# Kernel optimization log

Hardware: AMD Instinct MI355X
Metric: run time of the kernel (lower is better)

## Reference

```python
import jax, jax.numpy as jnp
import numpy as np

N0, N1, N2 = 100000, 25000, 6250
E0, E1, E2 = 1600000, 400000, 100000
K = 6
NUM_CLASSES = 40


def cheb_conv(x, edge_index, W, b, num_nodes):
    # PyG ChebConv, normalization='sym', lambda_max=2.0:
    # L_hat = (2/lambda_max) * (I - D^-1/2 A D^-1/2) - I = -D^-1/2 A D^-1/2
    row, col = edge_index[0], edge_index[1]
    deg = jax.ops.segment_sum(jnp.ones(row.shape[0], x.dtype), row, num_segments=num_nodes)
    dinv = jnp.where(deg > 0, 1.0 / jnp.sqrt(jnp.maximum(deg, 1e-12)), 0.0)
    norm = -(dinv[row] * dinv[col])  # per-edge weight of L_hat

    def Lhat(v):  # [N, F] -> [N, F], sparse gather + scatter-add
        return jax.ops.segment_sum(norm[:, None] * v[col], row, num_segments=num_nodes)

    Tx0 = x
    out = Tx0 @ W[0]
    Tx1 = Lhat(x)
    out = out + Tx1 @ W[1]
    for k in range(2, W.shape[0]):  # Chebyshev recurrence T_k = 2 L_hat T_{k-1} - T_{k-2}
        Tx2 = 2.0 * Lhat(Tx1) - Tx0
        out = out + Tx2 @ W[k]
        Tx0, Tx1 = Tx1, Tx2
    return out + b


def spmm_pool(row, col, values, n_out, h):
    # torch_sparse.spmm(indices, values, size0, size1, h)
    return jax.ops.segment_sum(values[:, None] * h[col], row, num_segments=n_out)


def setup_inputs() -> dict:
    key = jax.random.key(0)
    ks = jax.random.split(key, 16)
    w = lambda k, shape: jax.random.normal(k, shape, jnp.float32) * 0.1
    return {
        "pos": jax.random.normal(ks[0], (N0, 3), jnp.float32),
        "edge_index0": jax.random.randint(ks[1], (2, E0), 0, N0),
        "edge_index1": jax.random.randint(ks[2], (2, E1), 0, N1),
        "edge_index2": jax.random.randint(ks[3], (2, E2), 0, N2),
        "ds0_row": jax.random.randint(ks[4], (N0,), 0, N1),
        "ds0_col": jax.random.randint(ks[5], (N0,), 0, N0),
        "ds0_values": jax.random.uniform(ks[6], (N0,), jnp.float32),
        "ds1_row": jax.random.randint(ks[7], (N1,), 0, N2),
        "ds1_col": jax.random.randint(ks[8], (N1,), 0, N1),
        "ds1_values": jax.random.uniform(ks[9], (N1,), jnp.float32),
        "W0": w(ks[10], (K, 3, 32)),  "b0": jnp.zeros((32,), jnp.float32),
        "W1": w(ks[11], (K, 32, 64)), "b1": jnp.zeros((64,), jnp.float32),
        "W2": w(ks[12], (K, 64, 128)),"b2": jnp.zeros((128,), jnp.float32),
        "Wh": w(ks[13], (128, 1024)), "bh": jnp.zeros((1024,), jnp.float32),
        "Wl": w(ks[14], (1024, NUM_CLASSES)), "bl": jnp.zeros((NUM_CLASSES,), jnp.float32),
    }


def reference(pos, edge_index0, edge_index1, edge_index2,
              ds0_row, ds0_col, ds0_values, ds1_row, ds1_col, ds1_values,
              W0, b0, W1, b1, W2, b2, Wh, bh, Wl, bl):
    h = jax.nn.relu(cheb_conv(pos, edge_index0, W0, b0, N0))
    h = spmm_pool(ds0_row, ds0_col, ds0_values, N1, h)
    h = jax.nn.relu(cheb_conv(h, edge_index1, W1, b1, N1))
    h = spmm_pool(ds1_row, ds1_col, ds1_values, N2, h)
    h = cheb_conv(h, edge_index2, W2, b2, N2)
    h = jnp.max(h @ Wh + bh, axis=0)  # global max pool over nodes
    return h @ Wl + bl  # [num_classes]
```

## Files before the change

### kernel.cpp

```cpp
#include <hip/hip_runtime.h>
#include <cstdint>
#include <cmath>

#define N0G 100000
#define N1G 25000
#define N2G 6250
#define E0G 1600000
#define E1G 400000
#define E2G 100000
#define KCH 6
#define NCLS 40
#define RPB 512
#define NBLK 240
#define PAYB 17
#define PAYM ((1u << PAYB) - 1u)
#define SCT 16
#define SCB (256 * SCT)
#define NST 5

static inline int cdiv(long a, long b){ return (int)((a + b - 1) / b); }

struct BP {
  const int* row[NST]; const int* col[NST]; const float* pval[NST];
  unsigned* ebuf[NST]; int* cs[NST]; float* wv[NST]; int* rp[NST]; float* dinv[NST];
  const float* xsrc[NST]; float4* xsdst[NST];
  int E[NST], N[NST], nbkt[NST], chunk[NST], ghoff[NST], pool[NST], nb[NST], bsumoff[NST];
  int blkS[NST + 1], blkB[NST + 1];
};

__global__ __launch_bounds__(256) void k_phist_b(BP p, int* __restrict__ gh){
  int s = blockIdx.x / NBLK, c = blockIdx.x % NBLK;
  const int* row = p.row[s];
  int E = p.E[s], nbkt = p.nbkt[s], chunk = p.chunk[s];
  int* g = gh + p.ghoff[s];
  __shared__ int h[256];
  for (int i = threadIdx.x; i < nbkt; i += 256) h[i] = 0;
  __syncthreads();
  int e0 = c * chunk, e1 = min(E, e0 + chunk);
  for (int e = e0 + threadIdx.x; e < e1; e += 256)
    atomicAdd(&h[row[e] >> 9], 1);
  __syncthreads();
  for (int i = threadIdx.x; i < nbkt; i += 256)
    g[i * NBLK + c] = h[i];
}

__global__ __launch_bounds__(256) void k_scanA_b(BP p, const int* __restrict__ gh, int* __restrict__ bsum){
  int s = 0; while (s < NST - 1 && (int)blockIdx.x >= p.blkS[s + 1]) s++;
  int lb = blockIdx.x - p.blkS[s];
  int M = p.nbkt[s] * NBLK;
  const int* g = gh + p.ghoff[s];
  __shared__ int sh[256];
  int base = lb * SCB + threadIdx.x * SCT;
  int su = 0;
#pragma unroll
  for (int j = 0; j < SCT; j++){ int i = base + j; if (i < M) su += g[i]; }
  sh[threadIdx.x] = su; __syncthreads();
  for (int o = 128; o > 0; o >>= 1){
    if (threadIdx.x < o) sh[threadIdx.x] += sh[threadIdx.x + o];
    __syncthreads();
  }
  if (threadIdx.x == 0) bsum[p.bsumoff[s] + lb] = sh[0];
}

__global__ __launch_bounds__(256) void k_scanC_b(BP p, int* __restrict__ gh, const int* __restrict__ bsum){
  int s = 0; while (s < NST - 1 && (int)blockIdx.x >= p.blkS[s + 1]) s++;
  int lb = blockIdx.x - p.blkS[s];
  int M = p.nbkt[s] * NBLK;
  int* g = gh + p.ghoff[s];
  __shared__ int sh[256];
  __shared__ int blockoff;
  if (threadIdx.x == 0){
    int off = 0;
    if (p.nb[s] > 1){
      const int* bs = bsum + p.bsumoff[s];
      for (int j = 0; j < lb; j++) off += bs[j];
    }
    blockoff = off;
  }
  int base = lb * SCB + threadIdx.x * SCT;
  int v[SCT]; int su = 0;
#pragma unroll
  for (int j = 0; j < SCT; j++){ int i = base + j; v[j] = (i < M) ? g[i] : 0; su += v[j]; }
  sh[threadIdx.x] = su;
  __syncthreads();
  for (int o = 1; o < 256; o <<= 1){
    int t = (threadIdx.x >= o) ? sh[threadIdx.x - o] : 0;
    __syncthreads();
    sh[threadIdx.x] += t;
    __syncthreads();
  }
  int excl = blockoff + sh[threadIdx.x] - su;
#pragma unroll
  for (int j = 0; j < SCT; j++){
    int i = base + j;
    if (i < M){ g[i] = excl; excl += v[j]; }
  }
  if (lb == 0 && threadIdx.x == 0) p.rp[s][p.N[s]] = p.E[s];
}

__global__ __launch_bounds__(256) void k_pscatter_b(BP p, const int* __restrict__ gh){
  int s = blockIdx.x / NBLK, c = blockIdx.x % NBLK;
  const int* row = p.row[s]; const int* col = p.col[s];
  int E = p.E[s], nbkt = p.nbkt[s], chunk = p.chunk[s], pool = p.pool[s];
  const int* g = gh + p.ghoff[s];
  unsigned* ebuf = p.ebuf[s];
  __shared__ int cur[256];
  for (int i = threadIdx.x; i < nbkt; i += 256) cur[i] = g[i * NBLK + c];
  __syncthreads();
  int e0 = c * chunk, e1 = min(E, e0 + chunk);
  for (int e = e0 + threadIdx.x; e < e1; e += 256){
    int r = row[e];
    int dst = atomicAdd(&cur[r >> 9], 1);
    unsigned pay = pool ? (unsigned)e : (unsigned)col[e];
    ebuf[dst] = ((unsigned)(r & 511) << PAYB) | pay;
  }
}

__global__ __launch_bounds__(512) void k_bfinal_b(BP p, const int* __restrict__ gh){
  int s = 0; while (s < NST - 1 && (int)blockIdx.x >= p.blkB[s + 1]) s++;
  int b = blockIdx.x - p.blkB[s];
  const int* g = gh + p.ghoff[s];
  const unsigned* ebuf = p.ebuf[s];
  int nbkt = p.nbkt[s], N = p.N[s], E = p.E[s], pool = p.pool[s];
  int* cs = p.cs[s]; float* wv = p.wv[s];
  int* rp = p.rp[s]; float* dinv = p.dinv[s];
  const int* pcol = p.col[s]; const float* pval = p.pval[s];
  __shared__ int h[512];
  __shared__ int cur[512];
  int e0 = g[b * NBLK];
  int e1 = (b + 1 < nbkt) ? g[(b + 1) * NBLK] : E;
  int r0 = b * RPB;
  int t = threadIdx.x;
  h[t] = 0;
  __syncthreads();
  for (int e = e0 + t; e < e1; e += 512)
    atomicAdd(&h[ebuf[e] >> PAYB], 1);
  __syncthreads();
  int cnt = h[t];
  __syncthreads();
  for (int o = 1; o < 512; o <<= 1){
    int tmp = (t >= o) ? h[t - o] : 0;
    __syncthreads();
    h[t] += tmp;
    __syncthreads();
  }
  int excl = h[t] - cnt;
  cur[t] = excl;
  int n = r0 + t;
  if (n < N){
    rp[n] = e0 + excl;
    if (!pool){
      float d = cnt > 0 ? rsqrtf((float)cnt) : 0.f;
      dinv[n] = d;
      if (p.xsrc[s]){
        const float* x = p.xsrc[s];
        p.xsdst[s][n] = make_float4(d * x[n * 3 + 0], d * x[n * 3 + 1], d * x[n * 3 + 2], 0.f);
      }
    }
  }
  __syncthreads();
  for (int e = e0 + t; e < e1; e += 512){
    unsigned u = ebuf[e];
    int pp = atomicAdd(&cur[u >> PAYB], 1);
    int dst = e0 + pp;
    if (pool){
      int ei = (int)(u & PAYM);
      cs[dst] = pcol[ei]; wv[dst] = pval[ei];
    } else {
      cs[dst] = (int)(u & PAYM);
    }
  }
}

__global__ __launch_bounds__(256) void k_gather3(const int* __restrict__ rp, const int* __restrict__ cs,
                          const float4* __restrict__ xs, const float* __restrict__ dinv,
                          const float* __restrict__ sub, float* __restrict__ dst,
                          float4* __restrict__ xs_out, int N, float scale){
  int tid = blockIdx.x * 256 + threadIdx.x;
  int n = tid >> 3, q = tid & 7;
  if (n >= N) return;
  int e0 = rp[n], e1 = rp[n + 1];
  float a0 = 0.f, a1 = 0.f, a2 = 0.f;
  for (int e = e0 + q; e < e1; e += 8){
    float4 v = xs[cs[e]];
    a0 += v.x; a1 += v.y; a2 += v.z;
  }
  a0 += __shfl_xor(a0, 1); a1 += __shfl_xor(a1, 1); a2 += __shfl_xor(a2, 1);
  a0 += __shfl_xor(a0, 2); a1 += __shfl_xor(a1, 2); a2 += __shfl_xor(a2, 2);
  a0 += __shfl_xor(a0, 4); a1 += __shfl_xor(a1, 4); a2 += __shfl_xor(a2, 4);
  if (q == 0){
    float dn = dinv[n];
    float m = -scale * dn;
    float r0 = m * a0, r1 = m * a1, r2 = m * a2;
    if (sub){ r0 -= sub[n * 3 + 0]; r1 -= sub[n * 3 + 1]; r2 -= sub[n * 3 + 2]; }
    dst[n * 3 + 0] = r0; dst[n * 3 + 1] = r1; dst[n * 3 + 2] = r2;
    if (xs_out) xs_out[n] = make_float4(dn * r0, dn * r1, dn * r2, 0.f);
  }
}

template<int F>
__global__ __launch_bounds__(256) void k_gatherT(const int* __restrict__ rp, const int* __restrict__ cs,
                          const float4* __restrict__ xs, const float* __restrict__ dinv,
                          const float* __restrict__ sub, float* __restrict__ dst,
                          float4* __restrict__ xs_out, int N, float scale){
  constexpr int L = F / 4;
  constexpr int G = 4 * L;
  int tid = blockIdx.x * 256 + threadIdx.x;
  int n = tid / G, q = tid % G;
  if (n >= N) return;
  int f4 = q % L, es = q / L;
  int e0 = rp[n], e1 = rp[n + 1];
  float4 acc = make_float4(0.f, 0.f, 0.f, 0.f);
  for (int e = e0 + es; e < e1; e += 4){
    float4 v = xs[(long)cs[e] * L + f4];
    acc.x += v.x; acc.y += v.y; acc.z += v.z; acc.w += v.w;
  }
  acc.x += __shfl_xor(acc.x, L);     acc.y += __shfl_xor(acc.y, L);
  acc.z += __shfl_xor(acc.z, L);     acc.w += __shfl_xor(acc.w, L);
  acc.x += __shfl_xor(acc.x, 2 * L); acc.y += __shfl_xor(acc.y, 2 * L);
  acc.z += __shfl_xor(acc.z, 2 * L); acc.w += __shfl_xor(acc.w, 2 * L);
  if (es == 0){
    float dn = dinv[n];
    float m = -scale * dn;
    float4 r = make_float4(m * acc.x, m * acc.y, m * acc.z, m * acc.w);
    if (sub){
      float4 sv = ((const float4*)sub)[(long)n * L + f4];
      r.x -= sv.x; r.y -= sv.y; r.z -= sv.z; r.w -= sv.w;
    }
    ((float4*)dst)[(long)n * L + f4] = r;
    if (xs_out) xs_out[(long)n * L + f4] = make_float4(dn * r.x, dn * r.y, dn * r.z, dn * r.w);
  }
}

template<int F>
__global__ __launch_bounds__(256) void k_gatherP(const int* __restrict__ rp, const int* __restrict__ cs,
                          const float* __restrict__ wv, const float* __restrict__ h,
                          float* __restrict__ dst, int N,
                          const float* __restrict__ dinvN, float4* __restrict__ xsN){
  constexpr int L = F / 4;
  int tid = blockIdx.x * 256 + threadIdx.x;
  int n = tid / L, q = tid % L;
  if (n >= N) return;
  const float4* h4 = (const float4*)h;
  int e0 = rp[n], e1 = rp[n + 1];
  float4 acc = make_float4(0.f, 0.f, 0.f, 0.f);
  for (int e = e0; e < e1; e++){
    int c = cs[e];
    float w = wv[e];
    float4 v = h4[(long)c * L + q];
    acc.x = fmaf(w, v.x, acc.x); acc.y = fmaf(w, v.y, acc.y);
    acc.z = fmaf(w, v.z, acc.z); acc.w = fmaf(w, v.w, acc.w);
  }
  ((float4*)dst)[(long)n * L + q] = acc;
  if (xsN){
    float dn = dinvN[n];
    xsN[(long)n * L + q] = make_float4(dn * acc.x, dn * acc.y, dn * acc.z, dn * acc.w);
  }
}

template<int F, int FO, int R, bool RELU>
__global__ __launch_bounds__(256) void k_cheb_tile(const float* __restrict__ x, const float* __restrict__ T, int N,
                           const float* __restrict__ W, const float* __restrict__ b,
                           float* __restrict__ out){
  constexpr int OQ4  = FO / 4;
  constexpr int NSUB = 256 / OQ4;
  constexpr int NT   = NSUB * R;
  constexpr int F6   = KCH * F;
  int n0 = blockIdx.x * NT;
  int o4   = threadIdx.x % OQ4;
  int nsub = threadIdx.x / OQ4;
  const float4* W4 = (const float4*)W;
  float4 acc[R];
  float4 bb = ((const float4*)b)[o4];
#pragma unroll
  for (int r = 0; r < R; r++) acc[r] = bb;

  if constexpr (F == 3){
    constexpr int PITCH = F6 + 2;
    __shared__ float X[NT * PITCH];
    for (int i = threadIdx.x; i < NT * F6; i += 256){
      int k = i / (NT * 3);
      int idx = i - k * (NT * 3);
      const float* src = (k == 0) ? x : (T + (size_t)(k - 1) * N * 3);
      int node = idx / 3, j = idx - node * 3;
      float v = (n0 + node < N) ? src[(long)n0 * 3 + idx] : 0.f;
      X[node * PITCH + k * 3 + j] = v;
    }
    __syncthreads();
#pragma unroll
    for (int f = 0; f < F6; f++){
      float4 w = W4[(long)f * OQ4 + o4];
#pragma unroll
      for (int r = 0; r < R; r++){
        float v = X[(nsub * R + r) * PITCH + f];
        acc[r].x = fmaf(v, w.x, acc[r].x); acc[r].y = fmaf(v, w.y, acc[r].y);
        acc[r].z = fmaf(v, w.z, acc[r].z); acc[r].w = fmaf(v, w.w, acc[r].w);
      }
    }
  } else {
    constexpr int L  = F / 4;
    constexpr int P4 = F6 / 4 + 1;
    __shared__ float4 X[NT * P4];
    for (int i = threadIdx.x; i < NT * KCH * L; i += 256){
      int k = i / (NT * L);
      int idx = i - k * (NT * L);
      int node = idx / L, q = idx - node * L;
      const float4* src4 = (const float4*)((k == 0) ? x : (T + (size_t)(k - 1) * N * F));
      float4 v = make_float4(0.f, 0.f, 0.f, 0.f);
      if (n0 + node < N) v = src4[(long)n0 * L + idx];
      X[node * P4 + k * L + q] = v;
    }
    __syncthreads();
#pragma unroll 4
    for (int f4 = 0; f4 < F6 / 4; f4++){
      float4 w0 = W4[(long)(4 * f4 + 0) * OQ4 + o4];
      float4 w1 = W4[(long)(4 * f4 + 1) * OQ4 + o4];
      float4 w2 = W4[(long)(4 * f4 + 2) * OQ4 + o4];
      float4 w3 = W4[(long)(4 * f4 + 3) * OQ4 + o4];
#pragma unroll
      for (int r = 0; r < R; r++){
        float4 hv = X[(nsub * R + r) * P4 + f4];
        acc[r].x = fmaf(hv.x, w0.x, acc[r].x); acc[r].y = fmaf(hv.x, w0.y, acc[r].y);
        acc[r].z = fmaf(hv.x, w0.z, acc[r].z); acc[r].w = fmaf(hv.x, w0.w, acc[r].w);
        acc[r].x = fmaf(hv.y, w1.x, acc[r].x); acc[r].y = fmaf(hv.y, w1.y, acc[r].y);
        acc[r].z = fmaf(hv.y, w1.z, acc[r].z); acc[r].w = fmaf(hv.y, w1.w, acc[r].w);
        acc[r].x = fmaf(hv.z, w2.x, acc[r].x); acc[r].y = fmaf(hv.z, w2.y, acc[r].y);
        acc[r].z = fmaf(hv.z, w2.z, acc[r].z); acc[r].w = fmaf(hv.z, w2.w, acc[r].w);
        acc[r].x = fmaf(hv.w, w3.x, acc[r].x); acc[r].y = fmaf(hv.w, w3.y, acc[r].y);
        acc[r].z = fmaf(hv.w, w3.z, acc[r].z); acc[r].w = fmaf(hv.w, w3.w, acc[r].w);
      }
    }
  }

#pragma unroll
  for (int r = 0; r < R; r++){
    int n = n0 + nsub * R + r;
    if (n < N){
      float4 o = acc[r];
      if (RELU){
        o.x = fmaxf(o.x, 0.f); o.y = fmaxf(o.y, 0.f);
        o.z = fmaxf(o.z, 0.f); o.w = fmaxf(o.w, 0.f);
      }
      ((float4*)out)[(long)n * OQ4 + o4] = o;
    }
  }
}

__device__ __forceinline__ unsigned fmap(float x){
  unsigned u = __float_as_uint(x);
  return (u & 0x80000000u) ? ~u : (u | 0x80000000u);
}
__device__ __forceinline__ float funmap(unsigned u){
  return (u & 0x80000000u) ? __uint_as_float(u ^ 0x80000000u) : __uint_as_float(~u);
}

#define NT 32
__global__ __launch_bounds__(256) void k_hidden_max(const float* __restrict__ h2, const float* __restrict__ Wh,
                             const float* __restrict__ bh, unsigned* __restrict__ maxed, int N){
  __shared__ float4 sW[128 * 32];
  __shared__ float4 sh4[NT * 32];
  const float4* Wh4 = (const float4*)Wh;
  int ob = blockIdx.x;
  for (int i = threadIdx.x; i < 128 * 32; i += 256){
    int f = i >> 5, ol = i & 31;
    sW[i] = Wh4[(long)f * 256 + ob * 32 + ol];
  }
  int o4l  = threadIdx.x & 31;
  int nsub = threadIdx.x >> 5;
  float4 mm = make_float4(-INFINITY, -INFINITY, -INFINITY, -INFINITY);
  int ntiles = (N + NT - 1) / NT;
  for (int nt = blockIdx.y; nt < ntiles; nt += gridDim.y){
    int n0 = nt * NT;
    __syncthreads();
    for (int i = threadIdx.x; i < NT * 32; i += 256){
      int n = i >> 5;
      float4 v = make_float4(0.f, 0.f, 0.f, 0.f);
      if (n0 + n < N) v = ((const float4*)h2)[(long)(n0 + n) * 32 + (i & 31)];
      sh4[i] = v;
    }
    __syncthreads();
    float4 acc[4];
#pragma unroll
    for (int j = 0; j < 4; j++) acc[j] = make_float4(0.f, 0.f, 0.f, 0.f);
#pragma unroll 4
    for (int f4 = 0; f4 < 32; f4++){
      float4 w0 = sW[(4 * f4 + 0) * 32 + o4l];
      float4 w1 = sW[(4 * f4 + 1) * 32 + o4l];
      float4 w2 = sW[(4 * f4 + 2) * 32 + o4l];
      float4 w3 = sW[(4 * f4 + 3) * 32 + o4l];
#pragma unroll
      for (int j = 0; j < 4; j++){
        float4 hv = sh4[(nsub * 4 + j) * 32 + f4];
        acc[j].x = fmaf(hv.x, w0.x, acc[j].x); acc[j].y = fmaf(hv.x, w0.y, acc[j].y);
        acc[j].z = fmaf(hv.x, w0.z, acc[j].z); acc[j].w = fmaf(hv.x, w0.w, acc[j].w);
        acc[j].x = fmaf(hv.y, w1.x, acc[j].x); acc[j].y = fmaf(hv.y, w1.y, acc[j].y);
        acc[j].z = fmaf(hv.y, w1.z, acc[j].z); acc[j].w = fmaf(hv.y, w1.w, acc[j].w);
        acc[j].x = fmaf(hv.z, w2.x, acc[j].x); acc[j].y = fmaf(hv.z, w2.y, acc[j].y);
        acc[j].z = fmaf(hv.z, w2.z, acc[j].z); acc[j].w = fmaf(hv.z, w2.w, acc[j].w);
        acc[j].x = fmaf(hv.w, w3.x, acc[j].x); acc[j].y = fmaf(hv.w, w3.y, acc[j].y);
        acc[j].z = fmaf(hv.w, w3.z, acc[j].z); acc[j].w = fmaf(hv.w, w3.w, acc[j].w);
      }
    }
#pragma unroll
    for (int j = 0; j < 4; j++){
      if (n0 + nsub * 4 + j < N){
        mm.x = fmaxf(mm.x, acc[j].x); mm.y = fmaxf(mm.y, acc[j].y);
        mm.z = fmaxf(mm.z, acc[j].z); mm.w = fmaxf(mm.w, acc[j].w);
      }
    }
  }
  __syncthreads();
  sh4[nsub * 32 + o4l] = mm;
  __syncthreads();
  if (nsub == 0){
#pragma unroll
    for (int s = 1; s < 8; s++){
      float4 o = sh4[s * 32 + o4l];
      mm.x = fmaxf(mm.x, o.x); mm.y = fmaxf(mm.y, o.y);
      mm.z = fmaxf(mm.z, o.z); mm.w = fmaxf(mm.w, o.w);
    }
    int o4 = ob * 32 + o4l;
    float4 b4 = ((const float4*)bh)[o4];
    atomicMax(&maxed[4 * o4 + 0], fmap(mm.x + b4.x));
    atomicMax(&maxed[4 * o4 + 1], fmap(mm.y + b4.y));
    atomicMax(&maxed[4 * o4 + 2], fmap(mm.z + b4.z));
    atomicMax(&maxed[4 * o4 + 3], fmap(mm.w + b4.w));
  }
}

__global__ __launch_bounds__(64) void k_final(const unsigned* __restrict__ maxed, const float* __restrict__ Wl,
                        const float* __restrict__ bl, float* __restrict__ out){
  int c = blockIdx.x;
  int l = threadIdx.x;
  float acc = 0.f;
  for (int o = l; o < 1024; o += 64)
    acc = fmaf(funmap(maxed[o]), Wl[o * NCLS + c], acc);
  for (int off = 32; off > 0; off >>= 1)
    acc += __shfl_down(acc, off);
  if (l == 0) out[c] = acc + bl[c];
}

template<int F, int FO, int R, bool RELU>
static void run_flowT(const int* rp, const int* cs, const float* dinv, int N,
                      const float* x, const float* W, const float* b, float* out,
                      float* T, float4* xin, float4* xout, hipStream_t s){
  const float* sub = nullptr; float scale = 1.f;
  const float* srcRaw = x;
  for (int k = 1; k < KCH; k++){
    float* Tk = T + (size_t)(k - 1) * N * F;
    float4* xo = (k == KCH - 1) ? nullptr : xout;
    k_gatherT<F><<<cdiv((long)N * F, 256), 256, 0, s>>>(rp, cs, xin, dinv, sub, Tk, xo, N, scale);
    sub = srcRaw; srcRaw = Tk; scale = 2.f;
    float4* t = xin; xin = xout; xout = t;
  }
  constexpr int NTC = (256 / (FO / 4)) * R;
  k_cheb_tile<F, FO, R, RELU><<<cdiv(N, NTC), 256, 0, s>>>(x, T, N, W, b, out);
}

extern "C" void kernel_launch(void* const* d_in, const int* in_sizes, int n_in,
                              void* d_out, int out_size, void* d_ws, size_t ws_size,
                              hipStream_t stream){
  const float* pos = (const float*)d_in[0];
  const int*   ei0 = (const int*)d_in[1];
  const int*   ei1 = (const int*)d_in[2];
  const int*   ei2 = (const int*)d_in[3];
  const int*   p0r = (const int*)d_in[4];
  const int*   p0c = (const int*)d_in[5];
  const float* p0v = (const float*)d_in[6];
  const int*   p1r = (const int*)d_in[7];
  const int*   p1c = (const int*)d_in[8];
  const float* p1v = (const float*)d_in[9];
  const float* W0  = (const float*)d_in[10]; const float* b0 = (const float*)d_in[11];
  const float* W1  = (const float*)d_in[12]; const float* b1 = (const float*)d_in[13];
  const float* W2  = (const float*)d_in[14]; const float* b2 = (const float*)d_in[15];
  const float* Wh  = (const float*)d_in[16]; const float* bh = (const float*)d_in[17];
  const float* Wl  = (const float*)d_in[18]; const float* bl = (const float*)d_in[19];
  float* out = (float*)d_out;

  float* TB = (float*)d_ws;
  float* hA = TB + 4000000;
  float* hB = hA + 3200000;
  float* hC = hB + 1600000;
  int* cs0   = (int*)(hC + 800000);
  int* cs1   = cs0 + 1600000;
  int* cs2   = cs1 + 400000;
  int* csP0  = cs2 + 100000;
  int* csP1  = csP0 + 100000;
  float* wvP0 = (float*)(csP1 + 25000);
  float* wvP1 = wvP0 + 100000;
  int* rp0  = (int*)(wvP1 + 25000);
  int* rp1  = rp0 + 100001;
  int* rp2  = rp1 + 25001;
  int* rpP0 = rp2 + 6251;
  int* rpP1 = rpP0 + 25001;
  float* dv0 = (float*)(rpP1 + 6251);
  float* dv1 = dv0 + 100000;
  float* dv2 = dv1 + 25000;
  int* gh   = (int*)(dv2 + 6250);
  int* bsum = gh + 76800;
  unsigned* maxed = (unsigned*)(bsum + 80);

  unsigned* eb0  = (unsigned*)TB;
  unsigned* eb1  = eb0 + 1600000;
  unsigned* eb2  = eb1 + 400000;
  unsigned* ebP0 = eb2 + 100000;
  unsigned* ebP1 = ebP0 + 100000;

  BP bp{};
  const int* rows[NST] = {ei0, ei1, ei2, p0r, p1r};
  const int* cols[NST] = {ei0 + E0G, ei1 + E1G, ei2 + E2G, p0c, p1c};
  const float* pvals[NST] = {nullptr, nullptr, nullptr, p0v, p1v};
  unsigned* ebufs[NST] = {eb0, eb1, eb2, ebP0, ebP1};
  int* css[NST] = {cs0, cs1, cs2, csP0, csP1};
  float* wvs[NST] = {nullptr, nullptr, nullptr, wvP0, wvP1};
  int* rps[NST] = {rp0, rp1, rp2, rpP0, rpP1};
  float* dvs[NST] = {dv0, dv1, dv2, nullptr, nullptr};
  int Es[NST] = {E0G, E1G, E2G, N0G, N1G};
  int Ns[NST] = {N0G, N1G, N2G, N1G, N2G};
  int pools[NST] = {0, 0, 0, 1, 1};
  int ghacc = 0, scanacc = 0, bacc = 0;
  bp.blkS[0] = 0; bp.blkB[0] = 0;
  for (int s = 0; s < NST; s++){
    bp.row[s] = rows[s]; bp.col[s] = cols[s]; bp.pval[s] = pvals[s];
    bp.ebuf[s] = ebufs[s]; bp.cs[s] = css[s]; bp.wv[s] = wvs[s];
    bp.rp[s] = rps[s]; bp.dinv[s] = dvs[s];
    bp.xsrc[s] = (s == 0) ? pos : nullptr;
    bp.xsdst[s] = (s == 0) ? (float4*)hB : nullptr;
    bp.E[s] = Es[s]; bp.N[s] = Ns[s]; bp.pool[s] = pools[s];
    bp.nbkt[s] = cdiv(Ns[s], RPB);
    bp.chunk[s] = cdiv(Es[s], NBLK);
    bp.ghoff[s] = ghacc; ghacc += bp.nbkt[s] * NBLK;
    bp.nb[s] = cdiv(bp.nbkt[s] * NBLK, SCB);
    bp.bsumoff[s] = s * 16;
    scanacc += bp.nb[s]; bp.blkS[s + 1] = scanacc;
    bacc += bp.nbkt[s]; bp.blkB[s + 1] = bacc;
  }

  k_phist_b<<<NST * NBLK, 256, 0, stream>>>(bp, gh);
  k_scanA_b<<<scanacc, 256, 0, stream>>>(bp, gh, bsum);
  k_scanC_b<<<scanacc, 256, 0, stream>>>(bp, gh, bsum);
  k_pscatter_b<<<NST * NBLK, 256, 0, stream>>>(bp, gh);
  k_bfinal_b<<<bacc, 512, 0, stream>>>(bp, gh);

  hipMemsetAsync(maxed, 0, 1024 * sizeof(unsigned), stream);

  {
    float4* xin = (float4*)hB; float4* xout = (float4*)(hB + 400000);
    const float* sub = nullptr; float scale = 1.f;
    const float* srcRaw = pos;
    for (int k = 1; k < KCH; k++){
      float* Tk = TB + (size_t)(k - 1) * N0G * 3;
      float4* xo = (k == KCH - 1) ? nullptr : xout;
      k_gather3<<<cdiv((long)N0G * 8, 256), 256, 0, stream>>>(rp0, cs0, xin, dv0, sub, Tk, xo, N0G, scale);
      sub = srcRaw; srcRaw = Tk; scale = 2.f;
      float4* t = xin; xin = xout; xout = t;
    }
    k_cheb_tile<3, 32, 2, true><<<cdiv(N0G, 64), 256, 0, stream>>>(pos, TB, N0G, W0, b0, hA);
  }

  k_gatherP<32><<<cdiv((long)N1G * 8, 256), 256, 0, stream>>>(rpP0, csP0, wvP0, hA, hC, N1G,
                                                              dv1, (float4*)hB);

  run_flowT<32, 64, 2, true>(rp1, cs1, dv1, N1G, hC, W1, b1, hA,
                             TB, (float4*)hB, (float4*)(hB + 800000), stream);

  k_gatherP<64><<<cdiv((long)N2G * 16, 256), 256, 0, stream>>>(rpP1, csP1, wvP1, hA, hC, N2G,
                                                               dv2, (float4*)hB);

  run_flowT<64, 128, 2, false>(rp2, cs2, dv2, N2G, hC, W2, b2, hA,
                               TB, (float4*)hB, (float4*)(hB + 400000), stream);

  dim3 g(8, 64);
  k_hidden_max<<<g, 256, 0, stream>>>(hA, Wh, bh, maxed, N2G);
  k_final<<<NCLS, 64, 0, stream>>>(maxed, Wl, bl, out);
}
```

Before: 355.9 us.

## Split hidden-layer max into per-tile partial max kernel plus reduction kernel

```diff
diff --git a/kernel.cpp b/kernel.cpp
--- a/kernel.cpp
+++ b/kernel.cpp
@@ -346,95 +346,91 @@
   }
 }
 
-__device__ __forceinline__ unsigned fmap(float x){
-  unsigned u = __float_as_uint(x);
-  return (u & 0x80000000u) ? ~u : (u | 0x80000000u);
-}
-__device__ __forceinline__ float funmap(unsigned u){
-  return (u & 0x80000000u) ? __uint_as_float(u ^ 0x80000000u) : __uint_as_float(~u);
-}
-
-#define NT 32
-__global__ __launch_bounds__(256) void k_hidden_max(const float* __restrict__ h2, const float* __restrict__ Wh,
-                             const float* __restrict__ bh, unsigned* __restrict__ maxed, int N){
-  __shared__ float4 sW[128 * 32];
-  __shared__ float4 sh4[NT * 32];
+#define HNT 8
+__global__ __launch_bounds__(256) void k_hidden1(const float* __restrict__ h2, const float* __restrict__ Wh,
+                                                 float4* __restrict__ pmax, int N){
+  __shared__ float4 sh4[HNT * 32];
+  int n0 = blockIdx.x * HNT;
+  for (int i = threadIdx.x; i < HNT * 32; i += 256){
+    int n = i >> 5;
+    float4 v = make_float4(0.f, 0.f, 0.f, 0.f);
+    if (n0 + n < N) v = ((const float4*)h2)[(long)(n0 + n) * 32 + (i & 31)];
+    sh4[i] = v;
+  }
+  __syncthreads();
+  int o4 = threadIdx.x;
   const float4* Wh4 = (const float4*)Wh;
-  int ob = blockIdx.x;
-  for (int i = threadIdx.x; i < 128 * 32; i += 256){
-    int f = i >> 5, ol = i & 31;
-    sW[i] = Wh4[(long)f * 256 + ob * 32 + ol];
-  }
-  int o4l  = threadIdx.x & 31;
-  int nsub = threadIdx.x >> 5;
-  float4 mm = make_float4(-INFINITY, -INFINITY, -INFINITY, -INFINITY);
-  int ntiles = (N + NT - 1) / NT;
-  for (int nt = blockIdx.y; nt < ntiles; nt += gridDim.y){
-    int n0 = nt * NT;
-    __syncthreads();
-    for (int i = threadIdx.x; i < NT * 32; i += 256){
-      int n = i >> 5;
-      float4 v = make_float4(0.f, 0.f, 0.f, 0.f);
-      if (n0 + n < N) v = ((const float4*)h2)[(long)(n0 + n) * 32 + (i & 31)];
-      sh4[i] = v;
-    }
-    __syncthreads();
-    float4 acc[4];
-#pragma unroll
-    for (int j = 0; j < 4; j++) acc[j] = make_float4(0.f, 0.f, 0.f, 0.f);
-#pragma unroll 4
-    for (int f4 = 0; f4 < 32; f4++){
-      float4 w0 = sW[(4 * f4 + 0) * 32 + o4l];
-      float4 w1 = sW[(4 * f4 + 1) * 32 + o4l];
-      float4 w2 = sW[(4 * f4 + 2) * 32 + o4l];
-      float4 w3 = sW[(4 * f4 + 3) * 32 + o4l];
-#pragma unroll
-      for (int j = 0; j < 4; j++){
-        float4 hv = sh4[(nsub * 4 + j) * 32 + f4];
-        acc[j].x = fmaf(hv.x, w0.x, acc[j].x); acc[j].y = fmaf(hv.x, w0.y, acc[j].y);
-        acc[j].z = fmaf(hv.x, w0.z, acc[j].z); acc[j].w = fmaf(hv.x, w0.w, acc[j].w);
-        acc[j].x = fmaf(hv.y, w1.x, acc[j].x); acc[j].y = fmaf(hv.y, w1.y, acc[j].y);
-        acc[j].z = fmaf(hv.y, w1.z, acc[j].z); acc[j].w = fmaf(hv.y, w1.w, acc[j].w);
-        acc[j].x = fmaf(hv.z, w2.x, acc[j].x); acc[j].y = fmaf(hv.z, w2.y, acc[j].y);
-        acc[j].z = fmaf(hv.z, w2.z, acc[j].z); acc[j].w = fmaf(hv.z, w2.w, acc[j].w);
-        acc[j].x = fmaf(hv.w, w3.x, acc[j].x); acc[j].y = fmaf(hv.w, w3.y, acc[j].y);
-        acc[j].z = fmaf(hv.w, w3.z, acc[j].z); acc[j].w = fmaf(hv.w, w3.w, acc[j].w);
-      }
-    }
-#pragma unroll
-    for (int j = 0; j < 4; j++){
-      if (n0 + nsub * 4 + j < N){
-        mm.x = fmaxf(mm.x, acc[j].x); mm.y = fmaxf(mm.y, acc[j].y);
-        mm.z = fmaxf(mm.z, acc[j].z); mm.w = fmaxf(mm.w, acc[j].w);
-      }
-    }
-  }
-  __syncthreads();
-  sh4[nsub * 32 + o4l] = mm;
-  __syncthreads();
-  if (nsub == 0){
-#pragma unroll
-    for (int s = 1; s < 8; s++){
-      float4 o = sh4[s * 32 + o4l];
-      mm.x = fmaxf(mm.x, o.x); mm.y = fmaxf(mm.y, o.y);
-      mm.z = fmaxf(mm.z, o.z); mm.w = fmaxf(mm.w, o.w);
-    }
-    int o4 = ob * 32 + o4l;
+  float4 acc[HNT];
+#pragma unroll
+  for (int j = 0; j < HNT; j++) acc[j] = make_float4(0.f, 0.f, 0.f, 0.f);
+#pragma unroll 2
+  for (int f4 = 0; f4 < 32; f4++){
+    float4 w0 = Wh4[(long)(4 * f4 + 0) * 256 + o4];
+    float4 w1 = Wh4[(long)(4 * f4 + 1) * 256 + o4];
+    float4 w2 = Wh4[(long)(4 * f4 + 2) * 256 + o4];
+    float4 w3 = Wh4[(long)(4 * f4 + 3) * 256 + o4];
+#pragma unroll
+    for (int j = 0; j < HNT; j++){
+      float4 hv = sh4[j * 32 + f4];
+      acc[j].x = fmaf(hv.x, w0.x, acc[j].x); acc[j].y = fmaf(hv.x, w0.y, acc[j].y);
+      acc[j].z = fmaf(hv.x, w0.z, acc[j].z); acc[j].w = fmaf(hv.x, w0.w, acc[j].w);
+      acc[j].x = fmaf(hv.y, w1.x, acc[j].x); acc[j].y = fmaf(hv.y, w1.y, acc[j].y);
+      acc[j].z = fmaf(hv.y, w1.z, acc[j].z); acc[j].w = fmaf(hv.y, w1.w, acc[j].w);
+      acc[j].x = fmaf(hv.z, w2.x, acc[j].x); acc[j].y = fmaf(hv.z, w2.y, acc[j].y);
+      acc[j].z = fmaf(hv.z, w2.z, acc[j].z); acc[j].w = fmaf(hv.z, w2.w, acc[j].w);
+      acc[j].x = fmaf(hv.w, w3.x, acc[j].x); acc[j].y = fmaf(hv.w, w3.y, acc[j].y);
+      acc[j].z = fmaf(hv.w, w3.z, acc[j].z); acc[j].w = fmaf(hv.w, w3.w, acc[j].w);
+    }
+  }
+  float4 m = make_float4(-INFINITY, -INFINITY, -INFINITY, -INFINITY);
+#pragma unroll
+  for (int j = 0; j < HNT; j++){
+    if (n0 + j < N){
+      m.x = fmaxf(m.x, acc[j].x); m.y = fmaxf(m.y, acc[j].y);
+      m.z = fmaxf(m.z, acc[j].z); m.w = fmaxf(m.w, acc[j].w);
+    }
+  }
+  pmax[(long)blockIdx.x * 256 + o4] = m;
+}
+
+__global__ __launch_bounds__(256) void k_hidden2(const float4* __restrict__ pmax, const float* __restrict__ bh,
+                                                 float* __restrict__ maxed, int nb){
+  __shared__ float4 red[256];
+  int lo4 = threadIdx.x & 7;
+  int rl  = threadIdx.x >> 3;
+  int o4  = blockIdx.x * 8 + lo4;
+  float4 m = make_float4(-INFINITY, -INFINITY, -INFINITY, -INFINITY);
+  for (int r = rl; r < nb; r += 32){
+    float4 v = pmax[(long)r * 256 + o4];
+    m.x = fmaxf(m.x, v.x); m.y = fmaxf(m.y, v.y);
+    m.z = fmaxf(m.z, v.z); m.w = fmaxf(m.w, v.w);
+  }
+  red[threadIdx.x] = m;
+  __syncthreads();
+  for (int off = 128; off >= 8; off >>= 1){
+    if (threadIdx.x < off){
+      float4 o = red[threadIdx.x + off];
+      float4 c = red[threadIdx.x];
+      c.x = fmaxf(c.x, o.x); c.y = fmaxf(c.y, o.y);
+      c.z = fmaxf(c.z, o.z); c.w = fmaxf(c.w, o.w);
+      red[threadIdx.x] = c;
+    }
+    __syncthreads();
+  }
+  if (threadIdx.x < 8){
+    float4 mm = red[threadIdx.x];
     float4 b4 = ((const float4*)bh)[o4];
-    atomicMax(&maxed[4 * o4 + 0], fmap(mm.x + b4.x));
-    atomicMax(&maxed[4 * o4 + 1], fmap(mm.y + b4.y));
-    atomicMax(&maxed[4 * o4 + 2], fmap(mm.z + b4.z));
-    atomicMax(&maxed[4 * o4 + 3], fmap(mm.w + b4.w));
-  }
-}
-
-__global__ __launch_bounds__(64) void k_final(const unsigned* __restrict__ maxed, const float* __restrict__ Wl,
+    ((float4*)maxed)[o4] = make_float4(mm.x + b4.x, mm.y + b4.y, mm.z + b4.z, mm.w + b4.w);
+  }
+}
+
+__global__ __launch_bounds__(64) void k_final(const float* __restrict__ maxed, const float* __restrict__ Wl,
                         const float* __restrict__ bl, float* __restrict__ out){
   int c = blockIdx.x;
   int l = threadIdx.x;
   float acc = 0.f;
   for (int o = l; o < 1024; o += 64)
-    acc = fmaf(funmap(maxed[o]), Wl[o * NCLS + c], acc);
+    acc = fmaf(maxed[o], Wl[o * NCLS + c], acc);
   for (int off = 32; off > 0; off >>= 1)
     acc += __shfl_down(acc, off);
   if (l == 0) out[c] = acc + bl[c];
@@ -498,7 +494,7 @@
   float* dv2 = dv1 + 25000;
   int* gh   = (int*)(dv2 + 6250);
   int* bsum = gh + 76800;
-  unsigned* maxed = (unsigned*)(bsum + 80);
+  float* maxed = (float*)(bsum + 80);
 
   unsigned* eb0  = (unsigned*)TB;
   unsigned* eb1  = eb0 + 1600000;
@@ -542,8 +538,6 @@
   k_pscatter_b<<<NST * NBLK, 256, 0, stream>>>(bp, gh);
   k_bfinal_b<<<bacc, 512, 0, stream>>>(bp, gh);
 
-  hipMemsetAsync(maxed, 0, 1024 * sizeof(unsigned), stream);
-
   {
     float4* xin = (float4*)hB; float4* xout = (float4*)(hB + 400000);
     const float* sub = nullptr; float scale = 1.f;
@@ -570,7 +564,10 @@
   run_flowT<64, 128, 2, false>(rp2, cs2, dv2, N2G, hC, W2, b2, hA,
                                TB, (float4*)hB, (float4*)(hB + 400000), stream);
 
-  dim3 g(8, 64);
-  k_hidden_max<<<g, 256, 0, stream>>>(hA, Wh, bh, maxed, N2G);
+  int nbH = cdiv(N2G, HNT);
+  float4* pmax = (float4*)TB;
+  k_hidden1<<<nbH, 256, 0, stream>>>(hA, Wh, pmax, N2G);
+  k_hidden2<<<32, 256, 0, stream>>>(pmax, bh, maxed, nbH);
+
   k_final<<<NCLS, 64, 0, stream>>>(maxed, Wl, bl, out);
 }
```

After: 352.1 us. No clear change (-1.1%).
